# Kernel optimization log

Hardware: AMD Instinct MI355X
Metric: run time of the kernel (lower is better)

Reference implementation:

```python
import jax, jax.numpy as jnp
import numpy as np

D_EMBED = 1024
D_QUERY = 512
NEG_INF = -1.0e9  # matches masked_fill value in the torch module


def setup_inputs() -> dict:
    key = jax.random.key(0)
    k_x, k_q, k_k, k_v, k_m = jax.random.split(key, 5)
    B, T = 8, 2048
    x = jax.random.normal(k_x, (B, T, D_EMBED), dtype=jnp.float32)
    # nn.Linear(d_embed, d_query, bias=False): y = x @ W^T; store W as (d_embed, d_query)
    sc = 1.0 / np.sqrt(D_EMBED)
    Wq = jax.random.normal(k_q, (D_EMBED, D_QUERY), dtype=jnp.float32) * sc
    Wk = jax.random.normal(k_k, (D_EMBED, D_QUERY), dtype=jnp.float32) * sc
    Wv = jax.random.normal(k_v, (D_EMBED, D_QUERY), dtype=jnp.float32) * sc
    attn_mask = jax.random.randint(k_m, (B, T), 0, 2).astype(jnp.bool_)
    return {"x": x, "Wq": Wq, "Wk": Wk, "Wv": Wv, "attn_mask": attn_mask}


def reference(x, Wq, Wk, Wv, attn_mask):
    # x: (B, T, d_embed)
    q = jnp.einsum("btd,dq->btq", x, Wq)  # (B, T, d_query)
    k = jnp.einsum("btd,dq->btq", x, Wk)
    v = jnp.einsum("btd,dq->btq", x, Wv)
    # NOTE: original module applies NO 1/sqrt(d) scaling.
    logits = jnp.einsum("btq,bsq->bts", q, k)  # (B, T, T)
    # attn_mask (B, T) broadcasts over the query axis: mask keys where mask is False
    logits = jnp.where(attn_mask[..., None, :], logits, NEG_INF)
    A = jax.nn.softmax(logits, axis=-1)
    return jnp.einsum("bts,bsq->btq", A, v)  # (B, T, d_query)
```

## Files before the change

kernel.cpp:

```cpp
#include <hip/hip_runtime.h>
#include <hip/hip_bf16.h>
#include <cstddef>
#include <cstdint>

#define BATCH 8
#define SEQ   2048
#define DEMB  1024
#define DQ    512

typedef __attribute__((ext_vector_type(8))) _Float16 f16x8;
typedef __attribute__((ext_vector_type(4))) float f32x4;

#define MFMA16(a, b, c) __builtin_amdgcn_mfma_f32_16x16x32_f16((a), (b), (c), 0, 0, 0)

#define GLDS16(gp, lp) __builtin_amdgcn_global_load_lds(                      \
    (const __attribute__((address_space(1))) void*)(gp),                      \
    (__attribute__((address_space(3))) void*)(lp), 16, 0, 0)

#define VM_BAR(N)                                                             \
  asm volatile("s_waitcnt vmcnt(" #N ")\n\ts_barrier" ::: "memory")
#define VM_LGKM_BAR(N)                                                        \
  asm volatile("s_waitcnt vmcnt(" #N ") lgkmcnt(0)\n\ts_barrier" ::: "memory")

__global__ __launch_bounds__(256) void prep_all(
    const float* __restrict__ x, _Float16* __restrict__ xh,
    const float* __restrict__ Wq, const float* __restrict__ Wk,
    const float* __restrict__ Wv, _Float16* __restrict__ wt,
    const int* __restrict__ maskg, int* __restrict__ pidx,
    int* __restrict__ cnt)
{
  const int bid = blockIdx.x;
  const int tid = threadIdx.x;

  if (bid < 8192) {
    size_t i = ((size_t)bid * 256 + tid) * 8;
    float4 a = *(const float4*)&x[i];
    float4 b = *(const float4*)&x[i + 4];
    f16x8 h;
    h[0] = (_Float16)a.x; h[1] = (_Float16)a.y;
    h[2] = (_Float16)a.z; h[3] = (_Float16)a.w;
    h[4] = (_Float16)b.x; h[5] = (_Float16)b.y;
    h[6] = (_Float16)b.z; h[7] = (_Float16)b.w;
    *(f16x8*)&xh[i] = h;
  } else if (bid < 9728) {
    int qidx = (bid - 8192) * 256 + tid;
    int w   = qidx >> 17;
    int rem = qidx & 131071;
    int k   = rem >> 7;
    int n   = (rem & 127) * 4;
    const float* W = (w == 0) ? Wq : (w == 1) ? Wk : Wv;
    float4 v = *(const float4*)&W[(size_t)k * DQ + n];
    _Float16* dst = wt + (size_t)w * (DQ * DEMB);
    dst[(size_t)(n + 0) * DEMB + k] = (_Float16)v.x;
    dst[(size_t)(n + 1) * DEMB + k] = (_Float16)v.y;
    dst[(size_t)(n + 2) * DEMB + k] = (_Float16)v.z;
    dst[(size_t)(n + 3) * DEMB + k] = (_Float16)v.w;
  } else {
    const int b = bid - 9728;
    __shared__ int tsum[256];
    int mv[8], s = 0;
    #pragma unroll
    for (int j = 0; j < 8; j++) {
      mv[j] = maskg[b * SEQ + tid * 8 + j];
      s += mv[j];
    }
    tsum[tid] = s;
    __syncthreads();
    for (int d = 1; d < 256; d <<= 1) {
      int v = (tid >= d) ? tsum[tid - d] : 0;
      __syncthreads();
      tsum[tid] += v;
      __syncthreads();
    }
    if (tid == 255) cnt[b] = tsum[255];
    int run = tsum[tid] - s;
    #pragma unroll
    for (int j = 0; j < 8; j++) {
      pidx[b * SEQ + tid * 8 + j] = mv[j] ? run : -1;
      run += mv[j];
    }
  }
}

__global__ __launch_bounds__(512) void proj_f16(
    const _Float16* __restrict__ xh, const _Float16* __restrict__ wt,
    const int* __restrict__ pidx,
    _Float16* __restrict__ kf, _Float16* __restrict__ vt,
    _Float16* __restrict__ qpack)
{
  const int w  = blockIdx.z;
  const int mt = blockIdx.y, nt = blockIdx.x;

  __shared__ _Float16 Xs[128][40];
  __shared__ _Float16 Ws[256][40];

  const int tid  = threadIdx.x;
  const int wave = tid >> 6, l = tid & 63;
  const int wm = wave >> 2;
  const int wn = wave & 3;
  const int lo4 = l & 15, hi2 = l >> 4;

  f32x4 acc[4][4];
  #pragma unroll
  for (int mf = 0; mf < 4; mf++)
    #pragma unroll
    for (int nf = 0; nf < 4; nf++)
      #pragma unroll
      for (int i = 0; i < 4; i++) acc[mf][nf][i] = 0.f;

  const int    xsrow = tid >> 2;
  const int    xskh  = (tid & 3) * 8;
  const size_t xbase = (size_t)(mt * 128 + xsrow) * DEMB + xskh;
  const int    wsrow = tid >> 1;
  const int    wskh  = (tid & 1) * 16;
  const size_t wbase = (size_t)w * (DQ * DEMB)
                     + (size_t)(nt * 256 + wsrow) * DEMB + wskh;

  #pragma unroll 1
  for (int k0 = 0; k0 < DEMB; k0 += 32) {
    *(f16x8*)&Xs[xsrow][xskh]    = *(const f16x8*)&xh[xbase + k0];
    *(f16x8*)&Ws[wsrow][wskh]    = *(const f16x8*)&wt[wbase + k0];
    *(f16x8*)&Ws[wsrow][wskh+8]  = *(const f16x8*)&wt[wbase + k0 + 8];
    __syncthreads();

    f16x8 a[4], bfr[4];
    #pragma unroll
    for (int mf = 0; mf < 4; mf++)
      a[mf] = *(const f16x8*)&Xs[wm*64 + mf*16 + lo4][hi2*8];
    #pragma unroll
    for (int nf = 0; nf < 4; nf++)
      bfr[nf] = *(const f16x8*)&Ws[wn*64 + nf*16 + lo4][hi2*8];
    #pragma unroll
    for (int mf = 0; mf < 4; mf++)
      #pragma unroll
      for (int nf = 0; nf < 4; nf++)
        acc[mf][nf] = MFMA16(a[mf], bfr[nf], acc[mf][nf]);
    __syncthreads();
  }

  const int mb = mt * 128 + wm * 64;
  const int nb = nt * 256 + wn * 64;
  #pragma unroll
  for (int mf = 0; mf < 4; mf++)
    #pragma unroll
    for (int nf = 0; nf < 4; nf++)
      #pragma unroll
      for (int i = 0; i < 4; i++) {
        int m = mb + mf*16 + hi2*4 + i;
        int n = nb + nf*16 + lo4;
        float val = acc[mf][nf][i];
        if (w == 0) {
          _Float16 h  = (_Float16)val;
          _Float16 lo = (_Float16)(val - (float)h);
          size_t base = (size_t)(m >> 6) * 65536 + (size_t)(m & 63) * 512 + n;
          qpack[base]         = h;
          qpack[base + 32768] = lo;
        } else if (w == 1) {
          int d_ = pidx[m];
          if (d_ >= 0)
            kf[((size_t)((m >> 11) << 11) + d_) * 512 + n] = (_Float16)val;
        } else {
          int d_ = pidx[m];
          if (d_ >= 0)
            vt[(size_t)(m >> 11) * (512 * 2048) + (size_t)n * 2048 + d_]
                = (_Float16)val;
        }
      }
}

__global__ __launch_bounds__(512, 2) void flash_v9(
    const _Float16* __restrict__ kfp, const _Float16* __restrict__ vtp,
    const int* __restrict__ cntg,
    float* dout)
{
  const int bb = blockIdx.x & 7;
  const int qt = blockIdx.x >> 3;
  const int q0 = qt * 64;

  const int tid = threadIdx.x;
  const int w = tid >> 6, l = tid & 63;
  const int qw = w & 3;
  const int kw = w >> 2;
  const int lo4 = l & 15, hi2 = l >> 4;

  __shared__ _Float16 Kst[2][64][256];
  __shared__ _Float16 Vst[2][256][64];
  __shared__ _Float16 P[64 * 64];
  __shared__ float pmax[2][64];

  const _Float16* qpk = (const _Float16*)dout + (size_t)(bb * 32 + qt) * 65536;
  const char*     kb  = (const char*)(kfp + (size_t)bb * SEQ * 512);
  const char*     vtb = (const char*)(vtp + (size_t)bb * (512 * 2048));

  const _Float16* qhi = qpk + (size_t)(qw * 16 + lo4) * 512;
  const _Float16* qlo = qhi + 32768;

  const int cnt = cntg[bb];
  const int nkt = (cnt + 63) >> 6;

#define STAGE_K(KT, H, B) do {                                                \
    const char* kg_ = kb + (size_t)(KT) * 64 * 1024;                          \
    char* lb_ = (char*)&Kst[(B)][0][0];                                       \
    _Pragma("unroll")                                                         \
    for (int i_ = 0; i_ < 4; i_++) {                                          \
      int D_ = i_ * 8192 + tid * 16;                                          \
      int row_ = D_ >> 9, cb_ = D_ & 511;                                     \
      GLDS16(kg_ + (size_t)row_ * 1024 + (H) * 512 +                          \
                 (cb_ ^ ((row_ & 7) << 4)),                                   \
             lb_ + D_);                                                       \
    } } while (0)

#define STAGE_V(KT, H, B) do {                                                \
    const char* vg_ = vtb + (size_t)(KT) * 128;                               \
    char* lb_ = (char*)&Vst[(B)][0][0];                                       \
    _Pragma("unroll")                                                         \
    for (int i_ = 0; i_ < 4; i_++) {                                          \
      int D_ = i_ * 8192 + tid * 16;                                          \
      int row_ = D_ >> 7, cb_ = D_ & 127;                                     \
      GLDS16(vg_ + (size_t)((H) * 256 + row_) * 4096 +                        \
                 (cb_ ^ ((row_ & 7) << 4)),                                   \
             lb_ + D_);                                                       \
    } } while (0)

#define QK_HALF(H, B) do {                                                    \
    const char* kl_ = (const char*)&Kst[(B)][0][0];                           \
    const int r0_ = kw * 32 + lo4, r1_ = r0_ + 16;                            \
    const int sw_ = (lo4 & 7) << 4;                                           \
    _Pragma("unroll")                                                         \
    for (int s_ = 0; s_ < 8; s_++) {                                          \
      const int dby_ = (s_ * 32 + hi2 * 8) * 2;                               \
      f16x8 k0 = *(const f16x8*)(kl_ + r0_ * 512 + (dby_ ^ sw_));             \
      f16x8 k1 = *(const f16x8*)(kl_ + r1_ * 512 + (dby_ ^ sw_));             \
      __builtin_amdgcn_s_setprio(1);                                          \
      S[0] = MFMA16(fq[(H) * 8 + s_], k0, S[0]);                              \
      S[1] = MFMA16(fq[(H) * 8 + s_], k1, S[1]);                              \
      S[0] = MFMA16(fql[(H) * 8 + s_], k0, S[0]);                             \
      S[1] = MFMA16(fql[(H) * 8 + s_], k1, S[1]);                             \
      __builtin_amdgcn_s_setprio(0);                                          \
    } } while (0)

#define PV_HALF(H, B) do {                                                    \
    const char* vl_ = (const char*)&Vst[(B)][0][0];                           \
    _Pragma("unroll")                                                         \
    for (int j_ = 0; j_ < 8; j_++) {                                          \
      const int dl_ = j_ * 32 + kw * 16 + lo4;                                \
      const int vs_ = (dl_ & 7) << 4;                                         \
      f16x8 v0 = *(const f16x8*)(vl_ + dl_ * 128 + ((hi2 * 16) ^ vs_));       \
      f16x8 v1 = *(const f16x8*)(vl_ + dl_ * 128 + ((64 + hi2 * 16) ^ vs_));  \
      __builtin_amdgcn_s_setprio(1);                                          \
      o[(H) * 8 + j_] = MFMA16(pa[0], v0, o[(H) * 8 + j_]);                   \
      o[(H) * 8 + j_] = MFMA16(pa[1], v1, o[(H) * 8 + j_]);                   \
      __builtin_amdgcn_s_setprio(0);                                          \
    } } while (0)

  f16x8 fq[16], fql[16];
  #pragma unroll
  for (int st = 0; st < 16; st++) {
    fq[st]  = *(const f16x8*)(qhi + st * 32 + hi2 * 8);
    fql[st] = *(const f16x8*)(qlo + st * 32 + hi2 * 8);
  }
  STAGE_K(0, 0, 0);
  __syncthreads();

  f32x4 o[16];
  #pragma unroll
  for (int f = 0; f < 16; f++)
    #pragma unroll
    for (int i = 0; i < 4; i++) o[f][i] = 0.f;
  f32x4 o_ones;
  #pragma unroll
  for (int i = 0; i < 4; i++) o_ones[i] = 0.f;

  f16x8 ones8;
  #pragma unroll
  for (int j = 0; j < 8; j++) ones8[j] = (_Float16)1.0f;

  float m_run[4], m_runP = -3.0e38f;
  #pragma unroll
  for (int i = 0; i < 4; i++) m_run[i] = -3.0e38f;

  const int ki0 = kw * 32 + lo4;
  const int ki1 = ki0 + 16;

  #pragma unroll 1
  for (int kt = 0; kt < nkt; kt++) {
    const int key0 = kt * 64;

    STAGE_K(kt, 1, 1);
    STAGE_V(kt, 0, 0);
    VM_BAR(8);

    f32x4 S[2];
    #pragma unroll
    for (int f = 0; f < 2; f++)
      #pragma unroll
      for (int i = 0; i < 4; i++) S[f][i] = 0.f;
    QK_HALF(0, 0);

    VM_BAR(4);
    QK_HALF(1, 1);

    STAGE_V(kt, 1, 1);
    STAGE_K(kt + 1, 0, 0);

    const bool t0 = (key0 + ki0 >= cnt);
    const bool t1 = (key0 + ki1 >= cnt);
    #pragma unroll
    for (int i = 0; i < 4; i++) {
      if (t0) S[0][i] = -1.0e9f;
      if (t1) S[1][i] = -1.0e9f;
      float mx = fmaxf(S[0][i], S[1][i]);
      #pragma unroll
      for (int off = 1; off < 16; off <<= 1)
        mx = fmaxf(mx, __shfl_xor(mx, off, 64));
      float p0 = __expf(S[0][i] - mx);
      float p1 = __expf(S[1][i] - mx);
      int row = qw*16 + hi2*4 + i;
      int swz = (row & 7) << 4;
      int b0  = (row*128 + (kw*32 + lo4)*2) ^ swz;
      int b1  = (row*128 + (kw*32 + 16 + lo4)*2) ^ swz;
      *(_Float16*)((char*)P + b0) = (_Float16)p0;
      *(_Float16*)((char*)P + b1) = (_Float16)p1;
      if (lo4 == 0) pmax[kw][row] = mx;
    }

    VM_LGKM_BAR(8);

    float oscale[4];
    #pragma unroll
    for (int i = 0; i < 4; i++) {
      int row = qw*16 + hi2*4 + i;
      float m0 = pmax[0][row], m1 = pmax[1][row];
      float mn = fmaxf(m_run[i], fmaxf(m0, m1));
      oscale[i] = __expf(m_run[i] - mn);
      m_run[i] = mn;
    }
    #pragma unroll
    for (int f = 0; f < 16; f++)
      #pragma unroll
      for (int i = 0; i < 4; i++) o[f][i] *= oscale[i];
    #pragma unroll
    for (int i = 0; i < 4; i++) o_ones[i] *= oscale[i];

    f16x8 pa[2];
    {
      const int prow = qw*16 + lo4;
      float m0p = pmax[0][prow], m1p = pmax[1][prow];
      float mnp = fmaxf(m_runP, fmaxf(m0p, m1p));
      m_runP = mnp;
      _Float16 c0 = (_Float16)__expf(m0p - mnp);
      _Float16 c1 = (_Float16)__expf(m1p - mnp);
      const int psw = (prow & 7) << 4;
      pa[0] = *(const f16x8*)((const char*)P + prow*128 + ((hi2*16) ^ psw));
      pa[1] = *(const f16x8*)((const char*)P + prow*128 + ((64 + hi2*16) ^ psw));
      pa[0] = pa[0] * c0;
      pa[1] = pa[1] * c1;
    }

    o_ones = MFMA16(pa[0], ones8, o_ones);
    o_ones = MFMA16(pa[1], ones8, o_ones);

    PV_HALF(0, 0);
    VM_BAR(4);
    PV_HALF(1, 1);
  }
#undef STAGE_K
#undef STAGE_V
#undef QK_HALF
#undef PV_HALF

  asm volatile("s_waitcnt vmcnt(0)" ::: "memory");

  #pragma unroll
  for (int i = 0; i < 4; i++) {
    float inv = 1.0f / o_ones[i];
    int rowg = bb * SEQ + q0 + qw*16 + hi2*4 + i;
    #pragma unroll
    for (int h = 0; h < 2; h++)
      #pragma unroll
      for (int j = 0; j < 8; j++) {
        int d = h*256 + j*32 + kw*16 + lo4;
        dout[(size_t)rowg * 512 + d] = o[h*8 + j][i] * inv;
      }
  }
}

extern "C" void kernel_launch(void* const* d_in, const int* in_sizes, int n_in,
                              void* d_out, int out_size, void* d_ws, size_t ws_size,
                              hipStream_t stream)
{
  const float* x    = (const float*)d_in[0];
  const float* Wq   = (const float*)d_in[1];
  const float* Wk   = (const float*)d_in[2];
  const float* Wv   = (const float*)d_in[3];
  const int*   mask = (const int*)d_in[4];

  _Float16* wsh = (_Float16*)d_ws;
  _Float16* KF = wsh;
  _Float16* VT = wsh +  8388608;
  _Float16* WT = wsh + 16777216;
  _Float16* XH = wsh + 18350080;
  int* PIDX    = (int*)(wsh + 35127296);
  int* CNT     = PIDX + 16384;

  prep_all<<<9736, 256, 0, stream>>>(x, XH, Wq, Wk, Wv, WT, mask, PIDX, CNT);

  dim3 pgrid(2, 128, 3);
  proj_f16<<<pgrid, 512, 0, stream>>>(XH, WT, PIDX, KF, VT, (_Float16*)d_out);

  flash_v9<<<256, 512, 0, stream>>>(KF, VT, CNT, (float*)d_out);
}
```

Measured before the change: 249.9 us.

## Fuse Q/K/V projections into one kernel sharing the X tile

The projection kernel now computes all three weight products (Q, K, V) in a single block, loading each X tile into shared memory once and reusing it across three weight tiles instead of launching a separate z-slice per weight. This removes the repeated X reads and cuts the grid to a third of its size. In exchange, each thread holds three times the accumulators (192 floats), which raises register pressure under launch_bounds(512,2), and the smaller grid may underfill the GPU.

```diff
diff --git a/kernel.cpp b/kernel.cpp
--- a/kernel.cpp
+++ b/kernel.cpp
@@ -82,17 +82,16 @@
   }
 }
 
-__global__ __launch_bounds__(512) void proj_f16(
+__global__ __launch_bounds__(512, 2) void proj3(
     const _Float16* __restrict__ xh, const _Float16* __restrict__ wt,
     const int* __restrict__ pidx,
     _Float16* __restrict__ kf, _Float16* __restrict__ vt,
     _Float16* __restrict__ qpack)
 {
-  const int w  = blockIdx.z;
   const int mt = blockIdx.y, nt = blockIdx.x;
 
   __shared__ _Float16 Xs[128][40];
-  __shared__ _Float16 Ws[256][40];
+  __shared__ _Float16 Ws[3][256][40];
 
   const int tid  = threadIdx.x;
   const int wave = tid >> 6, l = tid & 63;
@@ -100,41 +99,50 @@
   const int wn = wave & 3;
   const int lo4 = l & 15, hi2 = l >> 4;
 
-  f32x4 acc[4][4];
-  #pragma unroll
-  for (int mf = 0; mf < 4; mf++)
-    #pragma unroll
-    for (int nf = 0; nf < 4; nf++)
-      #pragma unroll
-      for (int i = 0; i < 4; i++) acc[mf][nf][i] = 0.f;
+  f32x4 acc[3][4][4];
+  #pragma unroll
+  for (int w = 0; w < 3; w++)
+    #pragma unroll
+    for (int mf = 0; mf < 4; mf++)
+      #pragma unroll
+      for (int nf = 0; nf < 4; nf++)
+        #pragma unroll
+        for (int i = 0; i < 4; i++) acc[w][mf][nf][i] = 0.f;
 
   const int    xsrow = tid >> 2;
   const int    xskh  = (tid & 3) * 8;
   const size_t xbase = (size_t)(mt * 128 + xsrow) * DEMB + xskh;
   const int    wsrow = tid >> 1;
   const int    wskh  = (tid & 1) * 16;
-  const size_t wbase = (size_t)w * (DQ * DEMB)
-                     + (size_t)(nt * 256 + wsrow) * DEMB + wskh;
+  const size_t wbase = (size_t)(nt * 256 + wsrow) * DEMB + wskh;
 
   #pragma unroll 1
   for (int k0 = 0; k0 < DEMB; k0 += 32) {
-    *(f16x8*)&Xs[xsrow][xskh]    = *(const f16x8*)&xh[xbase + k0];
-    *(f16x8*)&Ws[wsrow][wskh]    = *(const f16x8*)&wt[wbase + k0];
-    *(f16x8*)&Ws[wsrow][wskh+8]  = *(const f16x8*)&wt[wbase + k0 + 8];
+    *(f16x8*)&Xs[xsrow][xskh] = *(const f16x8*)&xh[xbase + k0];
+    #pragma unroll
+    for (int w = 0; w < 3; w++) {
+      const size_t wb = (size_t)w * (DQ * DEMB) + wbase + k0;
+      *(f16x8*)&Ws[w][wsrow][wskh]     = *(const f16x8*)&wt[wb];
+      *(f16x8*)&Ws[w][wsrow][wskh + 8] = *(const f16x8*)&wt[wb + 8];
+    }
     __syncthreads();
 
-    f16x8 a[4], bfr[4];
+    f16x8 a[4];
     #pragma unroll
     for (int mf = 0; mf < 4; mf++)
       a[mf] = *(const f16x8*)&Xs[wm*64 + mf*16 + lo4][hi2*8];
     #pragma unroll
-    for (int nf = 0; nf < 4; nf++)
-      bfr[nf] = *(const f16x8*)&Ws[wn*64 + nf*16 + lo4][hi2*8];
-    #pragma unroll
-    for (int mf = 0; mf < 4; mf++)
+    for (int w = 0; w < 3; w++) {
+      f16x8 bfr[4];
       #pragma unroll
       for (int nf = 0; nf < 4; nf++)
-        acc[mf][nf] = MFMA16(a[mf], bfr[nf], acc[mf][nf]);
+        bfr[nf] = *(const f16x8*)&Ws[w][wn*64 + nf*16 + lo4][hi2*8];
+      #pragma unroll
+      for (int mf = 0; mf < 4; mf++)
+        #pragma unroll
+        for (int nf = 0; nf < 4; nf++)
+          acc[w][mf][nf] = MFMA16(a[mf], bfr[nf], acc[w][mf][nf]);
+    }
     __syncthreads();
   }
 
@@ -148,22 +156,20 @@
       for (int i = 0; i < 4; i++) {
         int m = mb + mf*16 + hi2*4 + i;
         int n = nb + nf*16 + lo4;
-        float val = acc[mf][nf][i];
-        if (w == 0) {
+        {
+          float val = acc[0][mf][nf][i];
           _Float16 h  = (_Float16)val;
           _Float16 lo = (_Float16)(val - (float)h);
           size_t base = (size_t)(m >> 6) * 65536 + (size_t)(m & 63) * 512 + n;
           qpack[base]         = h;
           qpack[base + 32768] = lo;
-        } else if (w == 1) {
-          int d_ = pidx[m];
-          if (d_ >= 0)
-            kf[((size_t)((m >> 11) << 11) + d_) * 512 + n] = (_Float16)val;
-        } else {
-          int d_ = pidx[m];
-          if (d_ >= 0)
-            vt[(size_t)(m >> 11) * (512 * 2048) + (size_t)n * 2048 + d_]
-                = (_Float16)val;
+        }
+        int d_ = pidx[m];
+        if (d_ >= 0) {
+          kf[((size_t)((m >> 11) << 11) + d_) * 512 + n]
+              = (_Float16)acc[1][mf][nf][i];
+          vt[(size_t)(m >> 11) * (512 * 2048) + (size_t)n * 2048 + d_]
+              = (_Float16)acc[2][mf][nf][i];
         }
       }
 }
@@ -405,8 +411,8 @@
 
   prep_all<<<9736, 256, 0, stream>>>(x, XH, Wq, Wk, Wv, WT, mask, PIDX, CNT);
 
-  dim3 pgrid(2, 128, 3);
-  proj_f16<<<pgrid, 512, 0, stream>>>(XH, WT, PIDX, KF, VT, (_Float16*)d_out);
+  dim3 pgrid(2, 128);
+  proj3<<<pgrid, 512, 0, stream>>>(XH, WT, PIDX, KF, VT, (_Float16*)d_out);
 
   flash_v9<<<256, 512, 0, stream>>>(KF, VT, CNT, (float*)d_out);
 }
```

Measured after the change: 243.3 us. 2.6% less time.
